# Kernel tuning notes

Measured on AMD Instinct MI355X. Metric: run time of the kernel, lower is better.

Reference implementation:

```python
import jax, jax.numpy as jnp
import numpy as np

HOPS = 3  # C[i].weight tied to A[i+1].weight -> HOPS+1 distinct tables E_0..E_HOPS


def setup_inputs() -> dict:
    key = jax.random.key(0)
    ks = jax.random.split(key, 10)
    B, M, K, E, G, V = 32, 2048, 4, 128, 128, 50000
    s = 1.0 / np.sqrt(E).astype(np.float32)
    context = jax.random.randint(ks[0], (B, M, K), 0, V)          # memory (triples)
    h_ = jax.random.normal(ks[1], (B, G), dtype=jnp.float32)      # prev GRU hidden
    y_ = jax.random.randint(ks[2], (B,), 0, V)                    # prev token
    emb = jax.random.normal(ks[3], (HOPS + 1, V, E), dtype=jnp.float32) * 0.1
    W_ih = jax.random.normal(ks[4], (3 * G, E), dtype=jnp.float32) * s
    W_hh = jax.random.normal(ks[5], (3 * G, G), dtype=jnp.float32) * s
    b_ih = jax.random.normal(ks[6], (3 * G,), dtype=jnp.float32) * s
    b_hh = jax.random.normal(ks[7], (3 * G,), dtype=jnp.float32) * s
    W_vocab = jax.random.normal(ks[8], (V, 2 * E), dtype=jnp.float32) * s
    b_vocab = jax.random.normal(ks[9], (V,), dtype=jnp.float32) * s
    return dict(context=context, h_=h_, y_=y_, emb=emb, W_ih=W_ih, W_hh=W_hh,
                b_ih=b_ih, b_hh=b_hh, W_vocab=W_vocab, b_vocab=b_vocab)


def gru_cell(x, h, W_ih, W_hh, b_ih, b_hh):
    # PyTorch GRU cell semantics (r, z, n gate order).
    gi = x @ W_ih.T + b_ih
    gh = h @ W_hh.T + b_hh
    i_r, i_z, i_n = jnp.split(gi, 3, axis=-1)
    h_r, h_z, h_n = jnp.split(gh, 3, axis=-1)
    r = jax.nn.sigmoid(i_r + h_r)
    z = jax.nn.sigmoid(i_z + h_z)
    n = jnp.tanh(i_n + r * h_n)
    return (1.0 - z) * n + z * h


def reference(context, h_, y_, emb, W_ih, W_hh, b_ih, b_hh, W_vocab, b_vocab):
    x = emb[0][y_]                                   # [B, E] A[0] embed of prev token
    h = gru_cell(x, h_, W_ih, W_hh, b_ih, b_hh)      # [B, G], G == E
    q = h
    o1 = None
    attn = None
    for hop in range(HOPS):
        mA = emb[hop][context].sum(axis=2)           # gather [B,M,K,E] -> sum over K -> [B,M,E]
        p = jnp.einsum('bme,be->bm', mA, q)          # attention scores over memory slots
        attn = jax.nn.softmax(p, axis=1)             # [B, M]
        mC = emb[hop + 1][context].sum(axis=2)       # C[hop] table (tied to A[hop+1])
        o = jnp.einsum('bm,bme->be', attn, mC)       # memory read [B, E]
        q = q + o
        if hop == 0:
            o1 = o
    logits = jnp.concatenate([h, o1], axis=1) @ W_vocab.T + b_vocab  # [B, V]
    p_vocab = jax.nn.softmax(logits, axis=1)
    return h, p_vocab, attn
```

## Files before the change

### kernel.cpp

```cpp
#include <hip/hip_runtime.h>
#include <math.h>

#define BB 32
#define MM 2048
#define KK 4
#define EE 128
#define GG 128
#define VV 50000

__global__ __launch_bounds__(384) void gru_kernel(
    const float* __restrict__ emb0,
    const int*   __restrict__ y,
    const float* __restrict__ hprev,
    const float* __restrict__ W_ih,
    const float* __restrict__ W_hh,
    const float* __restrict__ b_ih,
    const float* __restrict__ b_hh,
    float* __restrict__ h_out,
    float* __restrict__ q,
    float* __restrict__ o1)
{
    int b = blockIdx.x;
    int t = threadIdx.x;
    __shared__ float x[EE], h[GG], gi[3*GG], gh[3*GG];
    if (t < EE)            x[t]       = emb0[(size_t)y[b]*EE + t];
    else if (t < 2*EE)     h[t-EE]    = hprev[b*GG + (t-EE)];
    if (t < EE) o1[b*EE + t] = 0.f;
    __syncthreads();
    {
        float accI = b_ih[t], accH = b_hh[t];
        const float* wi = W_ih + (size_t)t*EE;
        const float* wh = W_hh + (size_t)t*GG;
        #pragma unroll 8
        for (int e = 0; e < EE; e++) { accI += x[e]*wi[e]; accH += h[e]*wh[e]; }
        gi[t] = accI; gh[t] = accH;
    }
    __syncthreads();
    if (t < GG) {
        float r = 1.f/(1.f + __expf(-(gi[t]        + gh[t])));
        float z = 1.f/(1.f + __expf(-(gi[GG+t]     + gh[GG+t])));
        float n = tanhf(gi[2*GG+t] + r*gh[2*GG+t]);
        float hn = (1.f - z)*n + z*h[t];
        h_out[b*GG + t] = hn;
        q[b*GG + t]     = hn;
    }
}

__global__ __launch_bounds__(256) void t_kernel(
    const float* __restrict__ q,
    const float* __restrict__ embT,
    float* __restrict__ t)
{
    __shared__ float Ut[EE][32];
    __shared__ float Wt[32][132];
    int tid = threadIdx.x;
    for (int i = tid; i < EE*32; i += 256) {
        int e = i >> 5, b = i & 31;
        Ut[e][b] = q[b*EE + e];
    }
    int vg = tid & 31;
    int bg = tid >> 5;
    int v0 = blockIdx.x * 128;
    float acc[4][4];
    #pragma unroll
    for (int i = 0; i < 4; i++)
        #pragma unroll
        for (int j = 0; j < 4; j++) acc[i][j] = 0.f;

    int vrow = tid >> 1;
    int half = tid & 1;
    const float* wrow = embT + (size_t)(v0 + vrow)*EE + half*16;
    bool vok = (v0 + vrow) < VV;

    for (int ec = 0; ec < EE; ec += 32) {
        __syncthreads();
        #pragma unroll
        for (int j = 0; j < 4; j++) {
            float4 w = make_float4(0.f, 0.f, 0.f, 0.f);
            if (vok) w = *(const float4*)(wrow + ec + j*4);
            int e0 = half*16 + j*4;
            Wt[e0+0][vrow] = w.x;
            Wt[e0+1][vrow] = w.y;
            Wt[e0+2][vrow] = w.z;
            Wt[e0+3][vrow] = w.w;
        }
        __syncthreads();
        #pragma unroll 8
        for (int e = 0; e < 32; e++) {
            float4 w = *(const float4*)(&Wt[e][vg*4]);
            float4 u = *(const float4*)(&Ut[ec + e][bg*4]);
            acc[0][0] += w.x*u.x; acc[0][1] += w.x*u.y; acc[0][2] += w.x*u.z; acc[0][3] += w.x*u.w;
            acc[1][0] += w.y*u.x; acc[1][1] += w.y*u.y; acc[1][2] += w.y*u.z; acc[1][3] += w.y*u.w;
            acc[2][0] += w.z*u.x; acc[2][1] += w.z*u.y; acc[2][2] += w.z*u.z; acc[2][3] += w.z*u.w;
            acc[3][0] += w.w*u.x; acc[3][1] += w.w*u.y; acc[3][2] += w.w*u.z; acc[3][3] += w.w*u.w;
        }
    }
    #pragma unroll
    for (int i = 0; i < 4; i++) {
        int v = v0 + vg*4 + i;
        if (v < VV) {
            #pragma unroll
            for (int j = 0; j < 4; j++)
                t[(size_t)(bg*4 + j)*VV + v] = acc[i][j];
        }
    }
}

__global__ __launch_bounds__(256) void scores_lookup_kernel(
    const float* __restrict__ t,
    const int*   __restrict__ ctx,
    float* __restrict__ p)
{
    int gid = blockIdx.x*256 + threadIdx.x;
    int b   = gid >> 11;
    const int4 c = *(const int4*)(ctx + (size_t)gid*KK);
    const float* tb = t + (size_t)b*VV;
    p[gid] = tb[c.x] + tb[c.y] + tb[c.z] + tb[c.w];
}

template<int SAVE_O1>
__global__ __launch_bounds__(256) void oacc_fused_kernel(
    const float* __restrict__ embT,
    const int*   __restrict__ ctx,
    const float* __restrict__ p,
    float* __restrict__ S_out,
    float* __restrict__ q,
    float* __restrict__ o1)
{
    int blk = blockIdx.x;
    int b = blk >> 5, s = blk & 31;
    int t = threadIdx.x;
    int w = t >> 6, lane = t & 63;

    const float* row = p + (size_t)b*MM;
    float v[8];
    float mx = -INFINITY;
    #pragma unroll
    for (int i = 0; i < 8; i++) { v[i] = row[t + i*256]; mx = fmaxf(mx, v[i]); }
    __shared__ float red[6];
    #pragma unroll
    for (int off = 32; off; off >>= 1) mx = fmaxf(mx, __shfl_down(mx, off));
    if (lane == 0) red[w] = mx;
    __syncthreads();
    if (t == 0) red[4] = fmaxf(fmaxf(red[0],red[1]), fmaxf(red[2],red[3]));
    __syncthreads();
    mx = red[4];
    float sum = 0.f;
    #pragma unroll
    for (int i = 0; i < 8; i++) sum += __expf(v[i] - mx);
    #pragma unroll
    for (int off = 32; off; off >>= 1) sum += __shfl_down(sum, off);
    __syncthreads();
    if (lane == 0) red[w] = sum;
    __syncthreads();
    if (t == 0) red[5] = 1.f / (red[0]+red[1]+red[2]+red[3]);
    __syncthreads();
    float rs = red[5];

    int m0 = s*64 + w*16;
    float ax = 0.f, ay = 0.f;
    for (int i = 0; i < 16; i++) {
        int m = m0 + i;
        float a = __expf(row[m] - mx) * rs;
        const int4 c = *(const int4*)(ctx + (size_t)(b*MM + m)*KK);
        float2 v0 = *(const float2*)(embT + (size_t)c.x*EE + lane*2);
        float2 v1 = *(const float2*)(embT + (size_t)c.y*EE + lane*2);
        float2 v2 = *(const float2*)(embT + (size_t)c.z*EE + lane*2);
        float2 v3 = *(const float2*)(embT + (size_t)c.w*EE + lane*2);
        float sx = v0.x + v1.x + v2.x + v3.x;
        float sy = v0.y + v1.y + v2.y + v3.y;
        *(float2*)(S_out + ((size_t)b*MM + m)*EE + lane*2) = make_float2(sx, sy);
        ax += a * sx;
        ay += a * sy;
    }
    __shared__ float acc_red[4][EE];
    acc_red[w][lane*2]   = ax;
    acc_red[w][lane*2+1] = ay;
    __syncthreads();
    if (t < EE) {
        float vv = acc_red[0][t] + acc_red[1][t] + acc_red[2][t] + acc_red[3][t];
        atomicAdd(&q[b*EE + t], vv);
        if (SAVE_O1) atomicAdd(&o1[b*EE + t], vv);
    }
}

__global__ __launch_bounds__(256) void scores_s_kernel(
    const float* __restrict__ S,
    const float* __restrict__ q,
    float* __restrict__ p)
{
    int gid  = blockIdx.x * 4 + (threadIdx.x >> 6);
    int lane = threadIdx.x & 63;
    int b    = gid >> 11;
    float2 sv = *(const float2*)(S + (size_t)gid*EE + lane*2);
    float2 qv = *(const float2*)(q + b*EE + lane*2);
    float acc = sv.x*qv.x + sv.y*qv.y;
    #pragma unroll
    for (int off = 32; off; off >>= 1) acc += __shfl_down(acc, off);
    if (lane == 0) p[gid] = acc;
}

__global__ __launch_bounds__(256) void softmax_m_kernel(
    const float* __restrict__ p,
    float* __restrict__ attn)
{
    int b = blockIdx.x, t = threadIdx.x;
    const float* row = p + (size_t)b*MM;
    float v[8];
    float mx = -INFINITY;
    #pragma unroll
    for (int i = 0; i < 8; i++) { v[i] = row[t + i*256]; mx = fmaxf(mx, v[i]); }
    __shared__ float red[6];
    int w = t >> 6, lane = t & 63;
    #pragma unroll
    for (int off = 32; off; off >>= 1) mx = fmaxf(mx, __shfl_down(mx, off));
    if (lane == 0) red[w] = mx;
    __syncthreads();
    if (t == 0) { float m2 = fmaxf(fmaxf(red[0],red[1]), fmaxf(red[2],red[3])); red[4] = m2; }
    __syncthreads();
    mx = red[4];
    float sum = 0.f;
    #pragma unroll
    for (int i = 0; i < 8; i++) { v[i] = __expf(v[i] - mx); sum += v[i]; }
    #pragma unroll
    for (int off = 32; off; off >>= 1) sum += __shfl_down(sum, off);
    if (lane == 0) red[w] = sum;
    __syncthreads();
    if (t == 0) { red[5] = 1.f / (red[0]+red[1]+red[2]+red[3]); }
    __syncthreads();
    float rs = red[5];
    #pragma unroll
    for (int i = 0; i < 8; i++) attn[(size_t)b*MM + t + i*256] = v[i]*rs;
}

__global__ __launch_bounds__(256) void logits_kernel(
    const float* __restrict__ h,
    const float* __restrict__ o1,
    const float* __restrict__ Wv,
    const float* __restrict__ bv,
    float* __restrict__ logits)
{
    __shared__ float Ut[256][32];
    __shared__ float Wt[32][132];
    int t = threadIdx.x;
    for (int i = t; i < 256*32; i += 256) {
        int e = i >> 5, b = i & 31;
        Ut[e][b] = (e < GG) ? h[b*GG + e] : o1[b*EE + (e - GG)];
    }
    int vg = t & 31;
    int bg = t >> 5;
    int v0 = blockIdx.x * 128;
    float acc[4][4];
    #pragma unroll
    for (int i = 0; i < 4; i++)
        #pragma unroll
        for (int j = 0; j < 4; j++) acc[i][j] = 0.f;

    int vrow = t >> 1;
    int half = t & 1;
    const float* wrow = Wv + (size_t)(v0 + vrow)*256 + half*16;
    bool vok = (v0 + vrow) < VV;

    for (int ec = 0; ec < 256; ec += 32) {
        __syncthreads();
        #pragma unroll
        for (int j = 0; j < 4; j++) {
            float4 w = make_float4(0.f, 0.f, 0.f, 0.f);
            if (vok) w = *(const float4*)(wrow + ec + j*4);
            int e0 = half*16 + j*4;
            Wt[e0+0][vrow] = w.x;
            Wt[e0+1][vrow] = w.y;
            Wt[e0+2][vrow] = w.z;
            Wt[e0+3][vrow] = w.w;
        }
        __syncthreads();
        #pragma unroll 8
        for (int e = 0; e < 32; e++) {
            float4 w = *(const float4*)(&Wt[e][vg*4]);
            float4 u = *(const float4*)(&Ut[ec + e][bg*4]);
            acc[0][0] += w.x*u.x; acc[0][1] += w.x*u.y; acc[0][2] += w.x*u.z; acc[0][3] += w.x*u.w;
            acc[1][0] += w.y*u.x; acc[1][1] += w.y*u.y; acc[1][2] += w.y*u.z; acc[1][3] += w.y*u.w;
            acc[2][0] += w.z*u.x; acc[2][1] += w.z*u.y; acc[2][2] += w.z*u.z; acc[2][3] += w.z*u.w;
            acc[3][0] += w.w*u.x; acc[3][1] += w.w*u.y; acc[3][2] += w.w*u.z; acc[3][3] += w.w*u.w;
        }
    }
    #pragma unroll
    for (int i = 0; i < 4; i++) {
        int v = v0 + vg*4 + i;
        if (v < VV) {
            float bb = bv[v];
            #pragma unroll
            for (int j = 0; j < 4; j++)
                logits[(size_t)(bg*4 + j)*VV + v] = acc[i][j] + bb;
        }
    }
}

#define VCHUNK 6250
__global__ __launch_bounds__(256) void vpart_kernel(
    const float* __restrict__ logits,
    float* __restrict__ part)
{
    int blk = blockIdx.x;
    int b = blk >> 3, c = blk & 7;
    int t = threadIdx.x;
    const float* row = logits + (size_t)b*VV;
    int start = c*VCHUNK;
    int end   = min(start + VCHUNK, VV);
    __shared__ float red[4];
    int w = t >> 6, lane = t & 63;
    float mx = -INFINITY;
    for (int i = start + t; i < end; i += 256) mx = fmaxf(mx, row[i]);
    #pragma unroll
    for (int off = 32; off; off >>= 1) mx = fmaxf(mx, __shfl_down(mx, off));
    if (lane == 0) red[w] = mx;
    __syncthreads();
    float m = fmaxf(fmaxf(red[0], red[1]), fmaxf(red[2], red[3]));
    float sum = 0.f;
    for (int i = start + t; i < end; i += 256) sum += __expf(row[i] - m);
    #pragma unroll
    for (int off = 32; off; off >>= 1) sum += __shfl_down(sum, off);
    __syncthreads();
    if (lane == 0) red[w] = sum;
    __syncthreads();
    if (t == 0) {
        part[blk*2]   = m;
        part[blk*2+1] = red[0] + red[1] + red[2] + red[3];
    }
}

__global__ __launch_bounds__(256) void vfinal_kernel(
    float* __restrict__ logits,
    const float* __restrict__ part)
{
    int i = blockIdx.x*256 + threadIdx.x;
    if (i >= BB*VV) return;
    int b = i / VV;
    const float* pp = part + b*16;
    float M = -INFINITY;
    #pragma unroll
    for (int c = 0; c < 8; c++) M = fmaxf(M, pp[c*2]);
    float S = 0.f;
    #pragma unroll
    for (int c = 0; c < 8; c++) S += pp[c*2+1] * __expf(pp[c*2] - M);
    logits[i] = __expf(logits[i] - M) * (1.f / S);
}

extern "C" void kernel_launch(void* const* d_in, const int* in_sizes, int n_in,
                              void* d_out, int out_size, void* d_ws, size_t ws_size,
                              hipStream_t stream) {
    const int*   ctx    = (const int*)  d_in[0];
    const float* h_prev = (const float*)d_in[1];
    const int*   y      = (const int*)  d_in[2];
    const float* emb    = (const float*)d_in[3];
    const float* W_ih   = (const float*)d_in[4];
    const float* W_hh   = (const float*)d_in[5];
    const float* b_ih   = (const float*)d_in[6];
    const float* b_hh   = (const float*)d_in[7];
    const float* Wv     = (const float*)d_in[8];
    const float* bv     = (const float*)d_in[9];

    float* out_h    = (float*)d_out;
    float* out_pv   = out_h + BB*GG;
    float* out_attn = out_pv + (size_t)BB*VV;

    float* ws   = (float*)d_ws;
    float* q    = ws;
    float* o1   = q + BB*EE;
    float* p    = o1 + BB*EE;
    float* tbuf = p + BB*MM;
    float* S1   = tbuf + (size_t)BB*VV;
    float* S2   = S1 + (size_t)BB*MM*EE;
    float* part = S2 + (size_t)BB*MM*EE;

    const float* e0 = emb;
    const float* e1 = emb + (size_t)1*VV*EE;
    const float* e2 = emb + (size_t)2*VV*EE;

    gru_kernel<<<BB, 384, 0, stream>>>(emb, y, h_prev, W_ih, W_hh, b_ih, b_hh, out_h, q, o1);

    t_kernel<<<391, 256, 0, stream>>>(q, e0, tbuf);
    scores_lookup_kernel<<<(BB*MM)/256, 256, 0, stream>>>(tbuf, ctx, p);
    oacc_fused_kernel<1><<<BB*32, 256, 0, stream>>>(e1, ctx, p, S1, q, o1);

    scores_s_kernel<<<(BB*MM)/4, 256, 0, stream>>>(S1, q, p);
    oacc_fused_kernel<0><<<BB*32, 256, 0, stream>>>(e2, ctx, p, S2, q, nullptr);

    scores_s_kernel<<<(BB*MM)/4, 256, 0, stream>>>(S2, q, p);
    softmax_m_kernel<<<BB, 256, 0, stream>>>(p, out_attn);

    logits_kernel<<<391, 256, 0, stream>>>(out_h, o1, Wv, bv, out_pv);
    vpart_kernel<<<BB*8, 256, 0, stream>>>(out_pv, part);
    vfinal_kernel<<<(BB*VV + 255)/256, 256, 0, stream>>>(out_pv, part);
}
```

Baseline: 320.4 us.

## Fuse vocab softmax partial stats into logits GEMM epilogue, drop vpart kernel

The logits GEMM now computes, for each 128-column tile, a per-row max and sum-exp in registers using warp shuffles, and writes them to a partial buffer. This removes the separate vpart kernel, which re-read the full 32x50000 logits. vfinal now merges 391 partials per row with an online-softmax tree reduction in shared memory, done per block. That adds redundant reduction work in each of its ~6250 blocks. An unroll pragma is also added to the oacc gather loop.

New measurement: 316.7 us. About the same (-1.1%).

```diff
diff --git a/kernel.cpp b/kernel.cpp
--- a/kernel.cpp
+++ b/kernel.cpp
@@ -7,6 +7,7 @@
 #define EE 128
 #define GG 128
 #define VV 50000
+#define NT 391
 
 __global__ __launch_bounds__(384) void gru_kernel(
     const float* __restrict__ emb0,
@@ -159,6 +160,7 @@
 
     int m0 = s*64 + w*16;
     float ax = 0.f, ay = 0.f;
+    #pragma unroll 4
     for (int i = 0; i < 16; i++) {
         int m = m0 + i;
         float a = __expf(row[m] - mx) * rs;
@@ -238,7 +240,8 @@
     const float* __restrict__ o1,
     const float* __restrict__ Wv,
     const float* __restrict__ bv,
-    float* __restrict__ logits)
+    float* __restrict__ logits,
+    float* __restrict__ part)
 {
     __shared__ float Ut[256][32];
     __shared__ float Wt[32][132];
@@ -259,14 +262,14 @@
     int vrow = t >> 1;
     int half = t & 1;
     const float* wrow = Wv + (size_t)(v0 + vrow)*256 + half*16;
-    bool vok = (v0 + vrow) < VV;
+    bool vrok = (v0 + vrow) < VV;
 
     for (int ec = 0; ec < 256; ec += 32) {
         __syncthreads();
         #pragma unroll
         for (int j = 0; j < 4; j++) {
             float4 w = make_float4(0.f, 0.f, 0.f, 0.f);
-            if (vok) w = *(const float4*)(wrow + ec + j*4);
+            if (vrok) w = *(const float4*)(wrow + ec + j*4);
             int e0 = half*16 + j*4;
             Wt[e0+0][vrow] = w.x;
             Wt[e0+1][vrow] = w.y;
@@ -287,45 +290,31 @@
     #pragma unroll
     for (int i = 0; i < 4; i++) {
         int v = v0 + vg*4 + i;
-        if (v < VV) {
-            float bb = bv[v];
-            #pragma unroll
-            for (int j = 0; j < 4; j++)
-                logits[(size_t)(bg*4 + j)*VV + v] = acc[i][j] + bb;
-        }
-    }
-}
-
-#define VCHUNK 6250
-__global__ __launch_bounds__(256) void vpart_kernel(
-    const float* __restrict__ logits,
-    float* __restrict__ part)
-{
-    int blk = blockIdx.x;
-    int b = blk >> 3, c = blk & 7;
-    int t = threadIdx.x;
-    const float* row = logits + (size_t)b*VV;
-    int start = c*VCHUNK;
-    int end   = min(start + VCHUNK, VV);
-    __shared__ float red[4];
-    int w = t >> 6, lane = t & 63;
-    float mx = -INFINITY;
-    for (int i = start + t; i < end; i += 256) mx = fmaxf(mx, row[i]);
-    #pragma unroll
-    for (int off = 32; off; off >>= 1) mx = fmaxf(mx, __shfl_down(mx, off));
-    if (lane == 0) red[w] = mx;
-    __syncthreads();
-    float m = fmaxf(fmaxf(red[0], red[1]), fmaxf(red[2], red[3]));
-    float sum = 0.f;
-    for (int i = start + t; i < end; i += 256) sum += __expf(row[i] - m);
-    #pragma unroll
-    for (int off = 32; off; off >>= 1) sum += __shfl_down(sum, off);
-    __syncthreads();
-    if (lane == 0) red[w] = sum;
-    __syncthreads();
-    if (t == 0) {
-        part[blk*2]   = m;
-        part[blk*2+1] = red[0] + red[1] + red[2] + red[3];
+        bool ok = v < VV;
+        float bb = ok ? bv[v] : 0.f;
+        #pragma unroll
+        for (int j = 0; j < 4; j++) {
+            float val = ok ? (acc[i][j] + bb) : -INFINITY;
+            acc[i][j] = val;
+            if (ok) logits[(size_t)(bg*4 + j)*VV + v] = val;
+        }
+    }
+    #pragma unroll
+    for (int j = 0; j < 4; j++) {
+        float m = fmaxf(fmaxf(acc[0][j], acc[1][j]), fmaxf(acc[2][j], acc[3][j]));
+        #pragma unroll
+        for (int off = 16; off; off >>= 1) m = fmaxf(m, __shfl_down(m, off, 32));
+        m = __shfl(m, 0, 32);
+        float s = 0.f;
+        #pragma unroll
+        for (int i = 0; i < 4; i++) s += __expf(acc[i][j] - m);
+        #pragma unroll
+        for (int off = 16; off; off >>= 1) s += __shfl_down(s, off, 32);
+        if (vg == 0) {
+            int b = bg*4 + j;
+            part[((size_t)b*NT + blockIdx.x)*2]     = m;
+            part[((size_t)b*NT + blockIdx.x)*2 + 1] = s;
+        }
     }
 }
 
@@ -333,17 +322,44 @@
     float* __restrict__ logits,
     const float* __restrict__ part)
 {
-    int i = blockIdx.x*256 + threadIdx.x;
-    if (i >= BB*VV) return;
-    int b = i / VV;
-    const float* pp = part + b*16;
-    float M = -INFINITY;
-    #pragma unroll
-    for (int c = 0; c < 8; c++) M = fmaxf(M, pp[c*2]);
-    float S = 0.f;
-    #pragma unroll
-    for (int c = 0; c < 8; c++) S += pp[c*2+1] * __expf(pp[c*2] - M);
-    logits[i] = __expf(logits[i] - M) * (1.f / S);
+    int i0  = blockIdx.x*256;
+    int tid = threadIdx.x;
+    int b0  = i0 / VV;
+    int last = min(i0 + 255, BB*VV - 1);
+    int bL  = last / VV;
+    __shared__ float redm[256], reds[256];
+    __shared__ float statM[2], statR[2];
+    for (int pass = 0; pass < 2; pass++) {
+        int b = b0 + pass;
+        if (b > bL) break;
+        float m = -INFINITY, s = 0.f;
+        for (int tt = tid; tt < NT; tt += 256) {
+            float pm = part[((size_t)b*NT + tt)*2];
+            float ps = part[((size_t)b*NT + tt)*2 + 1];
+            float M2 = fmaxf(m, pm);
+            s = s*__expf(m - M2) + ps*__expf(pm - M2);
+            m = M2;
+        }
+        redm[tid] = m; reds[tid] = s;
+        __syncthreads();
+        for (int off = 128; off; off >>= 1) {
+            if (tid < off) {
+                float m2 = redm[tid+off], s2 = reds[tid+off];
+                float M2 = fmaxf(redm[tid], m2);
+                reds[tid] = reds[tid]*__expf(redm[tid]-M2) + s2*__expf(m2-M2);
+                redm[tid] = M2;
+            }
+            __syncthreads();
+        }
+        if (tid == 0) { statM[pass] = redm[0]; statR[pass] = 1.f / reds[0]; }
+        __syncthreads();
+    }
+    int i = i0 + tid;
+    if (i < BB*VV) {
+        int b = i / VV;
+        int pass = b - b0;
+        logits[i] = __expf(logits[i] - statM[pass]) * statR[pass];
+    }
 }
 
 extern "C" void kernel_launch(void* const* d_in, const int* in_sizes, int n_in,
@@ -379,7 +395,7 @@
 
     gru_kernel<<<BB, 384, 0, stream>>>(emb, y, h_prev, W_ih, W_hh, b_ih, b_hh, out_h, q, o1);
 
-    t_kernel<<<391, 256, 0, stream>>>(q, e0, tbuf);
+    t_kernel<<<NT, 256, 0, stream>>>(q, e0, tbuf);
     scores_lookup_kernel<<<(BB*MM)/256, 256, 0, stream>>>(tbuf, ctx, p);
     oacc_fused_kernel<1><<<BB*32, 256, 0, stream>>>(e1, ctx, p, S1, q, o1);
 
@@ -389,7 +405,6 @@
     scores_s_kernel<<<(BB*MM)/4, 256, 0, stream>>>(S2, q, p);
     softmax_m_kernel<<<BB, 256, 0, stream>>>(p, out_attn);
 
-    logits_kernel<<<391, 256, 0, stream>>>(out_h, o1, Wv, bv, out_pv);
-    vpart_kernel<<<BB*8, 256, 0, stream>>>(out_pv, part);
+    logits_kernel<<<NT, 256, 0, stream>>>(out_h, o1, Wv, bv, out_pv, part);
     vfinal_kernel<<<(BB*VV + 255)/256, 256, 0, stream>>>(out_pv, part);
 }
```
